# Performance work log

Hardware: AMD Instinct MI355X
Metric: run time of the kernel (lower is better)

## Reference

```python
import jax, jax.numpy as jnp
import numpy as np

B, C, H, W = 8, 512, 64, 64
GH, GW = 240, 240  # hardcoded grid size in the source (240*240*2 slice)


def bilinear_grid_sample(x, grid):
    """F.grid_sample equivalent: bilinear, zeros padding, align_corners=True
    (old-PyTorch default used by this repo).
    x: [b, c, H, W], grid: [b, Hg, Wg, 2] with (x, y) normalized coords in [-1, 1].
    """
    b, c, h, w = x.shape
    hg, wg = grid.shape[1], grid.shape[2]
    ix = (grid[..., 0] + 1.0) * 0.5 * (w - 1)  # unnormalize, align_corners=True
    iy = (grid[..., 1] + 1.0) * 0.5 * (h - 1)
    ix0 = jnp.floor(ix)
    iy0 = jnp.floor(iy)
    ix1 = ix0 + 1.0
    iy1 = iy0 + 1.0
    wx1 = ix - ix0
    wx0 = 1.0 - wx1
    wy1 = iy - iy0
    wy0 = 1.0 - wy1
    xf = x.transpose(0, 2, 3, 1).reshape(b, h * w, c)  # [b, HW, c]

    def gather(iy_, ix_):
        m = (iy_ >= 0) & (iy_ <= h - 1) & (ix_ >= 0) & (ix_ <= w - 1)
        iyc = jnp.clip(iy_, 0, h - 1).astype(jnp.int32)
        ixc = jnp.clip(ix_, 0, w - 1).astype(jnp.int32)
        idx = (iyc * w + ixc).reshape(b, hg * wg, 1)
        v = jnp.take_along_axis(xf, idx, axis=1).reshape(b, hg, wg, c)
        return v * m[..., None].astype(x.dtype)

    out = (gather(iy0, ix0) * (wy0 * wx0)[..., None]
           + gather(iy0, ix1) * (wy0 * wx1)[..., None]
           + gather(iy1, ix0) * (wy1 * wx0)[..., None]
           + gather(iy1, ix1) * (wy1 * wx1)[..., None])
    return out.transpose(0, 3, 1, 2)  # [b, c, Hg, Wg]


def _identity_grid(b, h, w, dtype):
    # GeometricTnf resize == grid_sample with identity affine grid (align_corners=True)
    ys = jnp.linspace(-1.0, 1.0, h, dtype=dtype)
    xs = jnp.linspace(-1.0, 1.0, w, dtype=dtype)
    gy, gx = jnp.meshgrid(ys, xs, indexing='ij')
    return jnp.broadcast_to(jnp.stack([gx, gy], axis=-1)[None], (b, h, w, 2))


def setup_inputs() -> dict:
    key = jax.random.key(0)
    # grid channels must hold normalized coords, so sample uniform in [-1, 1]
    data = jax.random.uniform(key, (B, C, H, W), dtype=jnp.float32, minval=-1.0, maxval=1.0)
    return {"data": data}


def reference(data) -> jnp.ndarray:
    b, c, h, w = data.shape
    x = data[:, :c - 256]            # [b, c-256, h, w]
    theta_aff = data[:, c - 256:c - 128]
    theta_aff_tps = data[:, c - 128:]
    g_aff = theta_aff.reshape(b, -1)[:, :GH * GW * 2].reshape(b, GH, GW, 2)
    g_tps = theta_aff_tps.reshape(b, -1)[:, :GH * GW * 2].reshape(b, GH, GW, 2)
    warped_aff = bilinear_grid_sample(x, g_aff)          # [b, cx, 240, 240]
    warped_aff_tps = bilinear_grid_sample(warped_aff, g_tps)  # [b, cx, 240, 240]
    resized = bilinear_grid_sample(warped_aff_tps, _identity_grid(b, h, w, data.dtype))
    return x + resized
```

## Files before the change

kernel.cpp:

```cpp
#include <hip/hip_runtime.h>
#include <hip/hip_fp16.h>

#define H 64
#define W 64
#define NPIX 4096
#define GHH 240
#define GWW 240
#define CB 512
#define CX 256
#define NT4  16

static __device__ __forceinline__ unsigned pk_wi(float w, unsigned idx) {
    unsigned ub = __float_as_uint(w);
    ub = (ub + 0x7fffu + ((ub >> 16) & 1u)) & 0xffff0000u;
    return ub | idx;
}
static __device__ __forceinline__ unsigned pk_f16(float a, float b) {
    __half2 h = __floats2half2_rn(a, b);
    return *reinterpret_cast<unsigned*>(&h);
}

__global__ __launch_bounds__(256)
void stencil_kernel(const float* __restrict__ data, uint4* __restrict__ st) {
    const int b   = blockIdx.x & 7;
    const int pix = (blockIdx.x >> 3) * 256 + threadIdx.x;
    const int oy = pix >> 6, ox = pix & 63;

    const float*  xbase = data + (size_t)b * CB * NPIX;
    const float2* gaff  = (const float2*)(xbase + (size_t)256 * NPIX);
    const float2* gtps  = (const float2*)(xbase + (size_t)384 * NPIX);
    uint4* stb = st + (size_t)b * NT4 * NPIX;

    const float fy  = ((float)oy / 63.0f) * 239.0f;
    const float fx  = ((float)ox / 63.0f) * 239.0f;
    const float fy0 = floorf(fy), fx0 = floorf(fx);
    const float wy1 = fy - fy0,  wx1 = fx - fx0;

#pragma unroll
    for (int t = 0; t < 4; ++t) {
        const int tty = t >> 1, ttx = t & 1;
        const float gyf = fy0 + (float)tty;
        const float gxf = fx0 + (float)ttx;
        float wt = (tty ? wy1 : 1.0f - wy1) * (ttx ? wx1 : 1.0f - wx1);
        if (gyf < 0.0f || gyf > 239.0f || gxf < 0.0f || gxf > 239.0f) wt = 0.0f;
        const int gyi = min(max((int)gyf, 0), GHH - 1);
        const int gxi = min(max((int)gxf, 0), GWW - 1);

        const float2 gt = gtps[gyi * GWW + gxi];
        const float sx  = (gt.x + 1.0f) * 0.5f * 239.0f;
        const float sy  = (gt.y + 1.0f) * 0.5f * 239.0f;
        const float sy0 = floorf(sy), sx0 = floorf(sx);
        const float wsy1 = sy - sy0,  wsx1 = sx - sx0;

#pragma unroll
        for (int s = 0; s < 4; ++s) {
            const int ssy = s >> 1, ssx = s & 1;
            const float ayf = sy0 + (float)ssy;
            const float axf = sx0 + (float)ssx;
            float ws = (ssy ? wsy1 : 1.0f - wsy1) * (ssx ? wsx1 : 1.0f - wsx1);
            if (ayf < 0.0f || ayf > 239.0f || axf < 0.0f || axf > 239.0f) ws = 0.0f;
            ws *= wt;
            const int ayi = min(max((int)ayf, 0), GHH - 1);
            const int axi = min(max((int)axf, 0), GWW - 1);

            const float2 ga = gaff[ayi * GWW + axi];
            const float qx  = (ga.x + 1.0f) * 0.5f * 63.0f;
            const float qy  = (ga.y + 1.0f) * 0.5f * 63.0f;
            const float qy0 = floorf(qy), qx0 = floorf(qx);
            const float wqy1 = qy - qy0,  wqx1 = qx - qx0;

            unsigned pk[4];
#pragma unroll
            for (int r = 0; r < 4; ++r) {
                const int rry = r >> 1, rrx = r & 1;
                const float byf = qy0 + (float)rry;
                const float bxf = qx0 + (float)rrx;
                float wr = (rry ? wqy1 : 1.0f - wqy1) * (rrx ? wqx1 : 1.0f - wqx1);
                if (byf < 0.0f || byf > 63.0f || bxf < 0.0f || bxf > 63.0f) wr = 0.0f;
                wr *= ws;
                const int byi = min(max((int)byf, 0), H - 1);
                const int bxi = min(max((int)bxf, 0), W - 1);
                pk[r] = pk_wi(wr, (unsigned)(byi * W + bxi));
            }
            stb[(size_t)(t * 4 + s) * NPIX + pix] = make_uint4(pk[0], pk[1], pk[2], pk[3]);
        }
    }
}

__global__ __launch_bounds__(1024, 8)
void gather_kernel(const float* __restrict__ data, const uint4* __restrict__ st,
                   float* __restrict__ out) {
    __shared__ uint4 xl[NPIX];
    const int tid  = threadIdx.x;
    const int b    = blockIdx.x & 7;
    const int cg   = (blockIdx.x >> 3) & 31;
    const int half = blockIdx.x >> 8;
    const int c0   = cg * 8;

    const float* xbase = data + (size_t)b * CB * NPIX;
    const float* xc    = xbase + (size_t)c0 * NPIX;

    {
        float4 va[8];
#pragma unroll
        for (int c = 0; c < 8; ++c)
            va[c] = ((const float4*)(xc + (size_t)c * NPIX))[tid];
#pragma unroll
        for (int k = 0; k < 4; ++k) {
            uint4 u;
            u.x = pk_f16(((const float*)&va[0])[k], ((const float*)&va[1])[k]);
            u.y = pk_f16(((const float*)&va[2])[k], ((const float*)&va[3])[k]);
            u.z = pk_f16(((const float*)&va[4])[k], ((const float*)&va[5])[k]);
            u.w = pk_f16(((const float*)&va[6])[k], ((const float*)&va[7])[k]);
            xl[tid * 4 + k] = u;
        }
    }
    __syncthreads();

    const uint4* stb = st + (size_t)b * NT4 * NPIX;

#pragma unroll
    for (int pg = 0; pg < 2; ++pg) {
        const int pix = half * 2048 + pg * 1024 + tid;
        float a0 = 0.f, a1 = 0.f, a2 = 0.f, a3 = 0.f;
        float a4 = 0.f, a5 = 0.f, a6 = 0.f, a7 = 0.f;

#pragma unroll 4
        for (int g = 0; g < NT4; ++g) {
            const uint4 s4 = stb[(size_t)g * NPIX + pix];
#pragma unroll
            for (int r = 0; r < 4; ++r) {
                const unsigned u = (&s4.x)[r];
                const float w = __uint_as_float(u & 0xffff0000u);
                const uint4 v = xl[u & 0xffffu];
                const __half2 h01 = *reinterpret_cast<const __half2*>(&v.x);
                const __half2 h23 = *reinterpret_cast<const __half2*>(&v.y);
                const __half2 h45 = *reinterpret_cast<const __half2*>(&v.z);
                const __half2 h67 = *reinterpret_cast<const __half2*>(&v.w);
                a0 = fmaf(w, __half2float(__low2half (h01)), a0);
                a1 = fmaf(w, __half2float(__high2half(h01)), a1);
                a2 = fmaf(w, __half2float(__low2half (h23)), a2);
                a3 = fmaf(w, __half2float(__high2half(h23)), a3);
                a4 = fmaf(w, __half2float(__low2half (h45)), a4);
                a5 = fmaf(w, __half2float(__high2half(h45)), a5);
                a6 = fmaf(w, __half2float(__low2half (h67)), a6);
                a7 = fmaf(w, __half2float(__high2half(h67)), a7);
            }
        }

        float* o = out + ((size_t)b * CX + c0) * NPIX + pix;
        o[0 * NPIX] = xc[0 * NPIX + pix] + a0;
        o[1 * NPIX] = xc[1 * NPIX + pix] + a1;
        o[2 * NPIX] = xc[2 * NPIX + pix] + a2;
        o[3 * NPIX] = xc[3 * NPIX + pix] + a3;
        o[4 * NPIX] = xc[4 * NPIX + pix] + a4;
        o[5 * NPIX] = xc[5 * NPIX + pix] + a5;
        o[6 * NPIX] = xc[6 * NPIX + pix] + a6;
        o[7 * NPIX] = xc[7 * NPIX + pix] + a7;
    }
}

__global__ __launch_bounds__(1024, 4)
void warp_resblock_mono(const float* __restrict__ data, float* __restrict__ out) {
    const int tid = threadIdx.x;
    const int b   = blockIdx.x & 7;
    const int cg  = blockIdx.x >> 3;
    const int c0  = cg * 8;

    const float*  xbase = data + (size_t)b * CB * NPIX;
    const float2* gaff  = (const float2*)(xbase + (size_t)256 * NPIX);
    const float2* gtps  = (const float2*)(xbase + (size_t)384 * NPIX);

    __shared__ float4 xa[NPIX];
    __shared__ float4 xb[NPIX];
    {
        const float4* xs = (const float4*)(xbase + (size_t)c0 * NPIX);
        float4 va[4], vb[4];
#pragma unroll
        for (int cc = 0; cc < 4; ++cc) va[cc] = xs[(size_t)cc * 1024 + tid];
#pragma unroll
        for (int cc = 0; cc < 4; ++cc) vb[cc] = xs[(size_t)(4 + cc) * 1024 + tid];
#pragma unroll
        for (int k = 0; k < 4; ++k) {
            const int pix = tid * 4 + k;
            xa[pix] = make_float4(((const float*)&va[0])[k], ((const float*)&va[1])[k],
                                  ((const float*)&va[2])[k], ((const float*)&va[3])[k]);
            xb[pix] = make_float4(((const float*)&vb[0])[k], ((const float*)&vb[1])[k],
                                  ((const float*)&vb[2])[k], ((const float*)&vb[3])[k]);
        }
    }
    __syncthreads();

    for (int pg = 0; pg < 4; ++pg) {
        const int pix = pg * 1024 + tid;
        const int oy = pix >> 6, ox = pix & 63;
        float a0 = 0.f, a1 = 0.f, a2 = 0.f, a3 = 0.f;
        float a4 = 0.f, a5 = 0.f, a6 = 0.f, a7 = 0.f;

        const float fy  = ((float)oy / 63.0f) * 239.0f;
        const float fx  = ((float)ox / 63.0f) * 239.0f;
        const float fy0 = floorf(fy), fx0 = floorf(fx);
        const float wy1 = fy - fy0,  wx1 = fx - fx0;

#pragma unroll
        for (int t = 0; t < 4; ++t) {
            const int tty = t >> 1, ttx = t & 1;
            const float gyf = fy0 + (float)tty;
            const float gxf = fx0 + (float)ttx;
            float wt = (tty ? wy1 : 1.0f - wy1) * (ttx ? wx1 : 1.0f - wx1);
            if (gyf < 0.0f || gyf > 239.0f || gxf < 0.0f || gxf > 239.0f) wt = 0.0f;
            const int gyi = min(max((int)gyf, 0), GHH - 1);
            const int gxi = min(max((int)gxf, 0), GWW - 1);
            const float2 gt = gtps[gyi * GWW + gxi];
            const float sx  = (gt.x + 1.0f) * 0.5f * 239.0f;
            const float sy  = (gt.y + 1.0f) * 0.5f * 239.0f;
            const float sy0 = floorf(sy), sx0 = floorf(sx);
            const float wsy1 = sy - sy0,  wsx1 = sx - sx0;
#pragma unroll
            for (int s = 0; s < 4; ++s) {
                const int ssy = s >> 1, ssx = s & 1;
                const float ayf = sy0 + (float)ssy;
                const float axf = sx0 + (float)ssx;
                float ws = (ssy ? wsy1 : 1.0f - wsy1) * (ssx ? wsx1 : 1.0f - wsx1);
                if (ayf < 0.0f || ayf > 239.0f || axf < 0.0f || axf > 239.0f) ws = 0.0f;
                ws *= wt;
                const int ayi = min(max((int)ayf, 0), GHH - 1);
                const int axi = min(max((int)axf, 0), GWW - 1);
                const float2 ga = gaff[ayi * GWW + axi];
                const float qx  = (ga.x + 1.0f) * 0.5f * 63.0f;
                const float qy  = (ga.y + 1.0f) * 0.5f * 63.0f;
                const float qy0 = floorf(qy), qx0 = floorf(qx);
                const float wqy1 = qy - qy0,  wqx1 = qx - qx0;
#pragma unroll
                for (int r = 0; r < 4; ++r) {
                    const int rry = r >> 1, rrx = r & 1;
                    const float byf = qy0 + (float)rry;
                    const float bxf = qx0 + (float)rrx;
                    float wr = (rry ? wqy1 : 1.0f - wqy1) * (rrx ? wqx1 : 1.0f - wqx1);
                    if (byf < 0.0f || byf > 63.0f || bxf < 0.0f || bxf > 63.0f) wr = 0.0f;
                    wr *= ws;
                    const int byi = min(max((int)byf, 0), H - 1);
                    const int bxi = min(max((int)bxf, 0), W - 1);
                    const int idx = byi * W + bxi;
                    const float4 pa = xa[idx];
                    const float4 pb = xb[idx];
                    a0 = fmaf(wr, pa.x, a0); a1 = fmaf(wr, pa.y, a1);
                    a2 = fmaf(wr, pa.z, a2); a3 = fmaf(wr, pa.w, a3);
                    a4 = fmaf(wr, pb.x, a4); a5 = fmaf(wr, pb.y, a5);
                    a6 = fmaf(wr, pb.z, a6); a7 = fmaf(wr, pb.w, a7);
                }
            }
        }
        const float4 ra = xa[pix];
        const float4 rb = xb[pix];
        float* o = out + ((size_t)b * CX + c0) * NPIX + pix;
        o[0 * NPIX] = ra.x + a0; o[1 * NPIX] = ra.y + a1;
        o[2 * NPIX] = ra.z + a2; o[3 * NPIX] = ra.w + a3;
        o[4 * NPIX] = rb.x + a4; o[5 * NPIX] = rb.y + a5;
        o[6 * NPIX] = rb.z + a6; o[7 * NPIX] = rb.w + a7;
    }
}

extern "C" void kernel_launch(void* const* d_in, const int* in_sizes, int n_in,
                              void* d_out, int out_size, void* d_ws, size_t ws_size,
                              hipStream_t stream) {
    (void)in_sizes; (void)n_in; (void)out_size;
    const float* data = (const float*)d_in[0];
    float* out = (float*)d_out;
    const size_t ws_needed = (size_t)8 * NT4 * NPIX * sizeof(uint4);

    if (ws_size >= ws_needed) {
        uint4* st = (uint4*)d_ws;
        hipLaunchKernelGGL(stencil_kernel, dim3(128), dim3(256), 0, stream, data, st);
        hipLaunchKernelGGL(gather_kernel, dim3(512), dim3(1024), 0, stream, data, st, out);
    } else {
        hipLaunchKernelGGL(warp_resblock_mono, dim3(256), dim3(1024), 0, stream, data, out);
    }
}
```

Measured before the change: 52.98 us.

## Prefetch stencil entries, repack weight/index as fp16 plus byte offset, smaller stencil blocks

The packed stencil word now holds an fp16 weight in the low half and a precomputed byte offset in the high half. This removes the index-to-address multiply and the bf16-style masking in the gather inner loop. The gather loop is fully unrolled with a three-deep software prefetch of stencil entries, and the residual loads are moved before the accumulation loop to overlap them with gather work. The stencil kernel also switches to 128-thread blocks over twice as many blocks. The fp16 weights change rounding relative to the previous truncated-fp32 weights, and the larger unroll adds register pressure.

```diff
diff --git a/kernel.cpp b/kernel.cpp
--- a/kernel.cpp
+++ b/kernel.cpp
@@ -11,19 +11,18 @@
 #define NT4  16
 
 static __device__ __forceinline__ unsigned pk_wi(float w, unsigned idx) {
-    unsigned ub = __float_as_uint(w);
-    ub = (ub + 0x7fffu + ((ub >> 16) & 1u)) & 0xffff0000u;
-    return ub | idx;
+    const unsigned short hw = __half_as_ushort(__float2half(w));
+    return ((idx * 16u) << 16) | (unsigned)hw;
 }
 static __device__ __forceinline__ unsigned pk_f16(float a, float b) {
     __half2 h = __floats2half2_rn(a, b);
     return *reinterpret_cast<unsigned*>(&h);
 }
 
-__global__ __launch_bounds__(256)
+__global__ __launch_bounds__(128)
 void stencil_kernel(const float* __restrict__ data, uint4* __restrict__ st) {
     const int b   = blockIdx.x & 7;
-    const int pix = (blockIdx.x >> 3) * 256 + threadIdx.x;
+    const int pix = (blockIdx.x >> 3) * 128 + threadIdx.x;
     const int oy = pix >> 6, ox = pix & 63;
 
     const float*  xbase = data + (size_t)b * CB * NPIX;
@@ -118,21 +117,33 @@
     __syncthreads();
 
     const uint4* stb = st + (size_t)b * NT4 * NPIX;
-
-#pragma unroll
+    const char*  xlb = (const char*)xl;
+
     for (int pg = 0; pg < 2; ++pg) {
         const int pix = half * 2048 + pg * 1024 + tid;
+
+        float res[8];
+#pragma unroll
+        for (int c = 0; c < 8; ++c) res[c] = xc[(size_t)c * NPIX + pix];
+
         float a0 = 0.f, a1 = 0.f, a2 = 0.f, a3 = 0.f;
         float a4 = 0.f, a5 = 0.f, a6 = 0.f, a7 = 0.f;
 
-#pragma unroll 4
+        uint4 s_c  = stb[(size_t)0 * NPIX + pix];
+        uint4 s_n1 = stb[(size_t)1 * NPIX + pix];
+        uint4 s_n2 = stb[(size_t)2 * NPIX + pix];
+
+#pragma unroll
         for (int g = 0; g < NT4; ++g) {
-            const uint4 s4 = stb[(size_t)g * NPIX + pix];
+            const uint4 s4 = s_c;
+            s_c = s_n1; s_n1 = s_n2;
+            if (g + 3 < NT4) s_n2 = stb[(size_t)(g + 3) * NPIX + pix];
+
 #pragma unroll
             for (int r = 0; r < 4; ++r) {
                 const unsigned u = (&s4.x)[r];
-                const float w = __uint_as_float(u & 0xffff0000u);
-                const uint4 v = xl[u & 0xffffu];
+                const float w = __half2float(__ushort_as_half((unsigned short)(u & 0xffffu)));
+                const uint4 v = *(const uint4*)(xlb + (u >> 16));
                 const __half2 h01 = *reinterpret_cast<const __half2*>(&v.x);
                 const __half2 h23 = *reinterpret_cast<const __half2*>(&v.y);
                 const __half2 h45 = *reinterpret_cast<const __half2*>(&v.z);
@@ -149,14 +160,14 @@
         }
 
         float* o = out + ((size_t)b * CX + c0) * NPIX + pix;
-        o[0 * NPIX] = xc[0 * NPIX + pix] + a0;
-        o[1 * NPIX] = xc[1 * NPIX + pix] + a1;
-        o[2 * NPIX] = xc[2 * NPIX + pix] + a2;
-        o[3 * NPIX] = xc[3 * NPIX + pix] + a3;
-        o[4 * NPIX] = xc[4 * NPIX + pix] + a4;
-        o[5 * NPIX] = xc[5 * NPIX + pix] + a5;
-        o[6 * NPIX] = xc[6 * NPIX + pix] + a6;
-        o[7 * NPIX] = xc[7 * NPIX + pix] + a7;
+        o[0 * NPIX] = res[0] + a0;
+        o[1 * NPIX] = res[1] + a1;
+        o[2 * NPIX] = res[2] + a2;
+        o[3 * NPIX] = res[3] + a3;
+        o[4 * NPIX] = res[4] + a4;
+        o[5 * NPIX] = res[5] + a5;
+        o[6 * NPIX] = res[6] + a6;
+        o[7 * NPIX] = res[7] + a7;
     }
 }
 
@@ -271,7 +282,7 @@
 
     if (ws_size >= ws_needed) {
         uint4* st = (uint4*)d_ws;
-        hipLaunchKernelGGL(stencil_kernel, dim3(128), dim3(256), 0, stream, data, st);
+        hipLaunchKernelGGL(stencil_kernel, dim3(256), dim3(128), 0, stream, data, st);
         hipLaunchKernelGGL(gather_kernel, dim3(512), dim3(1024), 0, stream, data, st, out);
     } else {
         hipLaunchKernelGGL(warp_resblock_mono, dim3(256), dim3(1024), 0, stream, data, out);
```

Result: faster. 42.81 us (-19.2%).
